# Optimization experiments

Measured on AMD Instinct MI355X. Metric: run time of the kernel, lower is better.

## Reference

```python
import jax, jax.numpy as jnp
import numpy as np

B, K, C, L = 16, 8, 64, 2048
OFFSET = 2.0  # self.offset in Coupling
EPS = 1e-7    # clamp for logit stability (flows' safe_log analogue)


def setup_inputs() -> dict:
    key = jax.random.key(0)
    ks = jax.random.split(key, 6)
    return {
        "x_change": jax.random.normal(ks[0], (B, C, L), jnp.float32),
        "a": jax.random.normal(ks[1], (B, C, L), jnp.float32),
        "b": jax.random.normal(ks[2], (B, C, L), jnp.float32),
        "pi": jax.random.normal(ks[3], (B, K, C, L), jnp.float32),
        "mu": jax.random.normal(ks[4], (B, K, C, L), jnp.float32),
        "s": jax.random.normal(ks[5], (B, K, C, L), jnp.float32) * 0.1,  # log-scales
        "sldj": jnp.zeros((B,), jnp.float32),
    }


def reference(x_change, a, b, pi, mu, s, sldj):
    # scale = sigmoid(a + offset) + (1 - sigmoid(offset))
    sig_off = 1.0 - jax.nn.sigmoid(jnp.float32(OFFSET))
    scale = jax.nn.sigmoid(a + OFFSET) + sig_off                      # [B,C,L]

    logpi = jax.nn.log_softmax(pi, axis=1)                            # [B,K,C,L]
    z = (x_change[:, None] - mu) * jnp.exp(-s)                        # [B,K,C,L]

    # logistic.mixture_log_cdf: logsumexp_k(log pi_k + log sigmoid(z_k))
    log_cdf = jax.scipy.special.logsumexp(logpi + jax.nn.log_sigmoid(z), axis=1)
    u = jnp.clip(jnp.exp(log_cdf), EPS, 1.0 - EPS)                    # [B,C,L]

    # logistic.inverse (forward): logit, with ldj = -log(u) - log(1-u)
    y = jnp.log(u) - jnp.log1p(-u)
    scale_ldj = -jnp.log(u) - jnp.log1p(-u)

    # logistic.mixture_log_pdf: logsumexp_k(log pi_k + z - s - 2 softplus(z))
    log_pdf = jax.scipy.special.logsumexp(
        logpi + z - s - 2.0 * jax.nn.softplus(z), axis=1)             # [B,C,L]

    sldj_out = sldj + jnp.sum(
        (log_pdf + scale_ldj + jnp.log(scale)).reshape(sldj.shape[0], -1), axis=-1)
    out = (y + b) * scale                                             # [B,C,L]
    return out, sldj_out
```

## Files before the change

kernel.cpp:

```cpp
#include <hip/hip_runtime.h>

#define BB 16
#define KK 8
#define CC 64
#define LL 2048

constexpr int CL = CC * LL;
constexpr int QUADS_PER_BATCH = CL / 4;
constexpr int NBLOCKS = (BB * QUADS_PER_BATCH) / 256;

#define SIG_OFF 0.11920292202211755f
#define LOG_EPS -16.11809565095832f

__device__ __forceinline__ float frcp(float x) { return __builtin_amdgcn_rcpf(x); }

__device__ __forceinline__ float get4(const float4& v, int e) {
    switch (e) {
        case 0: return v.x;
        case 1: return v.y;
        case 2: return v.z;
        default: return v.w;
    }
}

__device__ __forceinline__ void set4(float4& v, int e, float f) {
    switch (e) {
        case 0: v.x = f; break;
        case 1: v.y = f; break;
        case 2: v.z = f; break;
        default: v.w = f; break;
    }
}

__global__ void init_sldj_kernel(const float* __restrict__ sldj_in,
                                 float* __restrict__ sldj_out) {
    int i = threadIdx.x;
    if (i < BB) sldj_out[i] = sldj_in[i];
}

__global__ __launch_bounds__(256, 2) void coupling_kernel(
    const float* __restrict__ x,
    const float* __restrict__ a,
    const float* __restrict__ bv,
    const float* __restrict__ pi,
    const float* __restrict__ mu,
    const float* __restrict__ s,
    float* __restrict__ out,
    float* __restrict__ sldj_out) {

    const int idx = blockIdx.x * 256 + threadIdx.x;
    const int b   = idx >> 15;
    const int rem = idx & (QUADS_PER_BATCH - 1);
    const int base = b * CL + rem * 4;

    const float4 x4 = *(const float4*)(x + base);
    const float4 a4 = *(const float4*)(a + base);
    const float4 b4 = *(const float4*)(bv + base);

    float4 pi4[KK], mu4[KK], s4[KK];
#pragma unroll
    for (int k = 0; k < KK; ++k) {
        const int kb = (b * KK + k) * CL + rem * 4;
        pi4[k] = *(const float4*)(pi + kb);
        mu4[k] = *(const float4*)(mu + kb);
        s4[k]  = *(const float4*)(s  + kb);
    }
    __builtin_amdgcn_sched_barrier(0);

    float Spi[4] = {0.f, 0.f, 0.f, 0.f};
    float Nc[4]  = {0.f, 0.f, 0.f, 0.f};
    float N1[4]  = {0.f, 0.f, 0.f, 0.f};
    float Np[4]  = {0.f, 0.f, 0.f, 0.f};

#pragma unroll
    for (int k = 0; k < KK; ++k) {
#pragma unroll
        for (int e = 0; e < 4; ++e) {
            const float p      = get4(pi4[k], e);
            const float m      = get4(mu4[k], e);
            const float sk     = get4(s4[k], e);
            const float invstd = __expf(-sk);
            const float z      = (get4(x4, e) - m) * invstd;

            const float t  = __expf(-fabsf(z));
            const float r  = frcp(1.f + t);
            const float tr = t * r;
            const float sig  = (z >= 0.f) ? r  : tr;
            const float osig = (z >= 0.f) ? tr : r;

            const float ek = __expf(p);
            Spi[e] += ek;
            Nc[e]  += ek * sig;
            N1[e]  += ek * osig;
            Np[e]  += ek * invstd * sig * osig;
        }
    }

    float contrib = 0.f;
    float4 out4;

#pragma unroll
    for (int e = 0; e < 4; ++e) {
        const float lSpi = __logf(Spi[e]);
        const float lu   = fmaxf(__logf(Nc[e]) - lSpi, LOG_EPS);
        const float lomu = fmaxf(__logf(N1[e]) - lSpi, LOG_EPS);
        const float y        = lu - lomu;
        const float ldj_term = -lu - lomu;
        const float log_pdf  = __logf(Np[e]) - lSpi;

        const float ae = get4(a4, e) + 2.f;
        const float t2 = __expf(-fabsf(ae));
        const float r2 = frcp(1.f + t2);
        const float sc = ((ae >= 0.f) ? r2 : t2 * r2) + SIG_OFF;

        set4(out4, e, (y + get4(b4, e)) * sc);
        contrib += log_pdf + ldj_term + __logf(sc);
    }

    *(float4*)(out + base) = out4;

#pragma unroll
    for (int off = 32; off > 0; off >>= 1)
        contrib += __shfl_down(contrib, off, 64);

    __shared__ float wsum[4];
    const int lane = threadIdx.x & 63;
    const int wid  = threadIdx.x >> 6;
    if (lane == 0) wsum[wid] = contrib;
    __syncthreads();
    if (threadIdx.x == 0) {
        atomicAdd(&sldj_out[b], wsum[0] + wsum[1] + wsum[2] + wsum[3]);
    }
}

extern "C" void kernel_launch(void* const* d_in, const int* in_sizes, int n_in,
                              void* d_out, int out_size, void* d_ws, size_t ws_size,
                              hipStream_t stream) {
    const float* x    = (const float*)d_in[0];
    const float* a    = (const float*)d_in[1];
    const float* bv   = (const float*)d_in[2];
    const float* pi   = (const float*)d_in[3];
    const float* mu   = (const float*)d_in[4];
    const float* s    = (const float*)d_in[5];
    const float* sldj = (const float*)d_in[6];

    float* out      = (float*)d_out;
    float* sldj_out = out + (size_t)BB * CL;

    init_sldj_kernel<<<1, 64, 0, stream>>>(sldj, sldj_out);
    coupling_kernel<<<NBLOCKS, 256, 0, stream>>>(x, a, bv, pi, mu, s, out, sldj_out);
}
```

Baseline: 224.4 us.

## Stream mixture parameters through an LDS ring with async global-to-LDS loads

Replaces the upfront register loads of all eight pi/mu/s float4 components with a 4-deep LDS ring buffer. The ring is filled by global_load_lds 16-byte async copies, and hand-placed vmcnt/lgkmcnt waits overlap later component loads with math on earlier ones. The aim is to cut register pressure, which drops the min-blocks launch bound and allows more waves in flight, while keeping many loads outstanding. In exchange it uses 48KB of LDS per block, which may cap occupancy. It also relies on exact waitcnt accounting that is fragile if the compiler reorders memory operations.

```diff
diff --git a/kernel.cpp b/kernel.cpp
--- a/kernel.cpp
+++ b/kernel.cpp
@@ -11,6 +11,8 @@
 
 #define SIG_OFF 0.11920292202211755f
 #define LOG_EPS -16.11809565095832f
+
+#define DEPTH 4
 
 __device__ __forceinline__ float frcp(float x) { return __builtin_amdgcn_rcpf(x); }
 
@@ -32,13 +34,20 @@
     }
 }
 
+__device__ __forceinline__ void glds16(const float* gsrc, const float* ldst) {
+    __builtin_amdgcn_global_load_lds(
+        (const __attribute__((address_space(1))) void*)gsrc,
+        (__attribute__((address_space(3))) void*)ldst,
+        16, 0, 0);
+}
+
 __global__ void init_sldj_kernel(const float* __restrict__ sldj_in,
                                  float* __restrict__ sldj_out) {
     int i = threadIdx.x;
     if (i < BB) sldj_out[i] = sldj_in[i];
 }
 
-__global__ __launch_bounds__(256, 2) void coupling_kernel(
+__global__ __launch_bounds__(256) void coupling_kernel(
     const float* __restrict__ x,
     const float* __restrict__ a,
     const float* __restrict__ bv,
@@ -48,22 +57,30 @@
     float* __restrict__ out,
     float* __restrict__ sldj_out) {
 
-    const int idx = blockIdx.x * 256 + threadIdx.x;
+    __shared__ float lds[DEPTH][3][1024];
+
+    const int tid = threadIdx.x;
+    const int idx = blockIdx.x * 256 + tid;
     const int b   = idx >> 15;
     const int rem = idx & (QUADS_PER_BATCH - 1);
     const int base = b * CL + rem * 4;
+    const int wid  = tid >> 6;
 
     const float4 x4 = *(const float4*)(x + base);
     const float4 a4 = *(const float4*)(a + base);
     const float4 b4 = *(const float4*)(bv + base);
+    __builtin_amdgcn_sched_barrier(0);
 
-    float4 pi4[KK], mu4[KK], s4[KK];
+    const int kb0 = (b * KK) * CL + rem * 4;
+    const float* pik = pi + kb0;
+    const float* muk = mu + kb0;
+    const float* svk = s  + kb0;
+
 #pragma unroll
-    for (int k = 0; k < KK; ++k) {
-        const int kb = (b * KK + k) * CL + rem * 4;
-        pi4[k] = *(const float4*)(pi + kb);
-        mu4[k] = *(const float4*)(mu + kb);
-        s4[k]  = *(const float4*)(s  + kb);
+    for (int k = 0; k < DEPTH; ++k) {
+        glds16(pik + k * CL, &lds[k][0][wid * 256]);
+        glds16(muk + k * CL, &lds[k][1][wid * 256]);
+        glds16(svk + k * CL, &lds[k][2][wid * 256]);
     }
     __builtin_amdgcn_sched_barrier(0);
 
@@ -74,11 +91,29 @@
 
 #pragma unroll
     for (int k = 0; k < KK; ++k) {
+        const int slot = k & (DEPTH - 1);
+
+        if (k <= 4)      asm volatile("s_waitcnt vmcnt(9)" ::: "memory");
+        else if (k == 5) asm volatile("s_waitcnt vmcnt(6)" ::: "memory");
+        else if (k == 6) asm volatile("s_waitcnt vmcnt(3)" ::: "memory");
+        else             asm volatile("s_waitcnt vmcnt(0)" ::: "memory");
+
+        const float4 p4 = *(const float4*)&lds[slot][0][tid * 4];
+        const float4 m4 = *(const float4*)&lds[slot][1][tid * 4];
+        const float4 s4 = *(const float4*)&lds[slot][2][tid * 4];
+
+        if (k < KK - DEPTH) {
+            asm volatile("s_waitcnt lgkmcnt(0)" ::: "memory");
+            glds16(pik + (k + DEPTH) * CL, &lds[slot][0][wid * 256]);
+            glds16(muk + (k + DEPTH) * CL, &lds[slot][1][wid * 256]);
+            glds16(svk + (k + DEPTH) * CL, &lds[slot][2][wid * 256]);
+        }
+
 #pragma unroll
         for (int e = 0; e < 4; ++e) {
-            const float p      = get4(pi4[k], e);
-            const float m      = get4(mu4[k], e);
-            const float sk     = get4(s4[k], e);
+            const float p      = get4(p4, e);
+            const float m      = get4(m4, e);
+            const float sk     = get4(s4, e);
             const float invstd = __expf(-sk);
             const float z      = (get4(x4, e) - m) * invstd;
 
@@ -124,11 +159,10 @@
         contrib += __shfl_down(contrib, off, 64);
 
     __shared__ float wsum[4];
-    const int lane = threadIdx.x & 63;
-    const int wid  = threadIdx.x >> 6;
+    const int lane = tid & 63;
     if (lane == 0) wsum[wid] = contrib;
     __syncthreads();
-    if (threadIdx.x == 0) {
+    if (tid == 0) {
         atomicAdd(&sldj_out[b], wsum[0] + wsum[1] + wsum[2] + wsum[3]);
     }
 }
```

Measured after the change: 221.7 us. No clear change (-1.2%).
